# Kernel tuning notes

Hardware: AMD Instinct MI355X
Metric: run time of the kernel (lower is better)

Reference implementation:

```python
import jax, jax.numpy as jnp
import numpy as np
import math

V, E, H, L, HID, T, B = 32000, 1024, 16, 4, 4096, 1024, 4
HS = E // H  # head size = 64


def _ln(x, g, b, eps=1e-5):
    m = jnp.mean(x, axis=-1, keepdims=True)
    v = jnp.var(x, axis=-1, keepdims=True)
    return (x - m) * jax.lax.rsqrt(v + eps) * g + b


def _pos_encoding(t, e):
    pos = jnp.arange(t, dtype=jnp.float32)[:, None]
    div = jnp.exp(jnp.arange(0, e, 2, dtype=jnp.float32) * (-math.log(10000.0) / e))
    pe = jnp.zeros((t, e), dtype=jnp.float32)
    pe = pe.at[:, 0::2].set(jnp.sin(pos * div))
    pe = pe.at[:, 1::2].set(jnp.cos(pos * div))
    return pe


def setup_inputs() -> dict:
    key = jax.random.key(0)
    ks = jax.random.split(key, 16)
    std = 0.02
    inp = {
        'idx': jax.random.randint(ks[0], (B, T), 0, V),
        'targets': jax.random.randint(ks[1], (B, T), 0, V),
        'tok_emb': jax.random.normal(ks[2], (V, E), jnp.float32) * std,
        'ln1_g': jnp.ones((L, E), jnp.float32),
        'ln1_b': jnp.zeros((L, E), jnp.float32),
        'wq': jax.random.normal(ks[3], (L, H, E, HS), jnp.float32) * std,
        'wk': jax.random.normal(ks[4], (L, H, E, HS), jnp.float32) * std,
        'wv': jax.random.normal(ks[5], (L, H, E, HS), jnp.float32) * std,
        'wo': jax.random.normal(ks[6], (L, H * HS, E), jnp.float32) * std,
        'bo': jnp.zeros((L, E), jnp.float32),
        'ln2_g': jnp.ones((L, E), jnp.float32),
        'ln2_b': jnp.zeros((L, E), jnp.float32),
        'w1': jax.random.normal(ks[7], (L, E, HID), jnp.float32) * std,
        'b1': jnp.zeros((L, HID), jnp.float32),
        'w2': jax.random.normal(ks[8], (L, HID, E), jnp.float32) * std,
        'b2': jnp.zeros((L, E), jnp.float32),
        'lnf_g': jnp.ones((E,), jnp.float32),
        'lnf_b': jnp.zeros((E,), jnp.float32),
        'lm_w': jax.random.normal(ks[9], (E, V), jnp.float32) * std,
        'lm_b': jnp.zeros((V,), jnp.float32),
    }
    return inp


def _forward(idx, targets, tok_emb, ln1_g, ln1_b, wq, wk, wv, wo, bo,
             ln2_g, ln2_b, w1, b1, w2, b2, lnf_g, lnf_b, lm_w, lm_b):
    b, t = idx.shape
    x = tok_emb[idx] * math.sqrt(E)              # [B,T,E], scaled embedding
    x = x + _pos_encoding(t, E)                  # sinusoidal pos enc
    causal = jnp.tril(jnp.ones((t, t), dtype=bool))
    scale = HS ** -0.5
    for l in range(L):
        h = _ln(x, ln1_g[l], ln1_b[l])
        q = jnp.einsum('bte,hek->bhtk', h, wq[l])
        k = jnp.einsum('bte,hek->bhtk', h, wk[l])
        v = jnp.einsum('bte,hek->bhtk', h, wv[l])
        scores = jnp.einsum('bhtk,bhsk->bhts', q, k) * scale
        scores = jnp.where(causal, scores, -jnp.inf)
        w = jax.nn.softmax(scores, axis=-1)
        o = jnp.einsum('bhts,bhsk->bhtk', w, v)
        o = o.transpose(0, 2, 1, 3).reshape(b, t, H * HS)  # concat heads
        x = x + o @ wo[l] + bo[l]
        h2 = _ln(x, ln2_g[l], ln2_b[l])
        x = x + jax.nn.relu(h2 @ w1[l] + b1[l]) @ w2[l] + b2[l]
    x = _ln(x, lnf_g, lnf_b)
    logits = x @ lm_w + lm_b                     # [B,T,V]
    logp = jax.nn.log_softmax(logits, axis=-1)
    loss = -jnp.mean(jnp.take_along_axis(logp, targets[..., None], axis=-1))
    return logits, loss


def reference(idx, targets, tok_emb, ln1_g, ln1_b, wq, wk, wv, wo, bo,
              ln2_g, ln2_b, w1, b1, w2, b2, lnf_g, lnf_b, lm_w, lm_b):
    return _forward(idx, targets, tok_emb, ln1_g, ln1_b, wq, wk, wv, wo, bo,
                    ln2_g, ln2_b, w1, b1, w2, b2, lnf_g, lnf_b, lm_w, lm_b)
```

## Files before the change

### kernel.cpp

```cpp
#include <hip/hip_runtime.h>
#include <hip/hip_bf16.h>
#include <math.h>

#define BB 4
#define TT 1024
#define BT 4096
#define EE 1024
#define HH 16
#define HSZ 64
#define LL 4
#define HID 4096
#define VV 32000
#define LOG2E 1.44269504f

typedef __attribute__((ext_vector_type(8))) __bf16 bf16x8;
typedef __attribute__((ext_vector_type(4))) float f32x4;

#define MFMA16(a, b, c) __builtin_amdgcn_mfma_f32_16x16x32_bf16((a), (b), (c), 0, 0, 0)

__device__ __forceinline__ int swz32(int row, int chunk) {
    return row * 32 + ((chunk ^ ((row >> 1) & 3)) << 3);
}

__device__ __forceinline__ void gload16(const __bf16* g, __bf16* l) {
    __builtin_amdgcn_global_load_lds(
        (const __attribute__((address_space(1))) unsigned int*)g,
        (__attribute__((address_space(3))) unsigned int*)l, 16, 0, 0);
}

__global__ __launch_bounds__(256) void transpose_conv(
    const float* __restrict__ in, __bf16* __restrict__ out,
    int R, int C, long ibs, int bdiv, long os1, long os2)
{
    __shared__ __bf16 tile[64][65];
    const int t = threadIdx.x;
    const int c0 = blockIdx.x * 64, r0 = blockIdx.y * 64;
    const int batch = blockIdx.z;
    const float* ib = in + (size_t)batch * ibs;
    __bf16* ob = out + (size_t)(batch / bdiv) * os1 + (size_t)(batch % bdiv) * os2;
#pragma unroll
    for (int p = 0; p < 4; ++p) {
        const int r = (t >> 4) + p * 16;
        const int c = (t & 15) * 4;
        float4 v = *(const float4*)(ib + (size_t)(r0 + r) * C + c0 + c);
        tile[c + 0][r] = (__bf16)v.x;
        tile[c + 1][r] = (__bf16)v.y;
        tile[c + 2][r] = (__bf16)v.z;
        tile[c + 3][r] = (__bf16)v.w;
    }
    __syncthreads();
#pragma unroll
    for (int p = 0; p < 2; ++p) {
        const int g = t + p * 256;
        const int co = g >> 3, ch = g & 7;
        bf16x8 vv;
#pragma unroll
        for (int j = 0; j < 8; ++j) vv[j] = tile[co][ch * 8 + j];
        *(bf16x8*)(ob + (size_t)(c0 + co) * R + r0 + ch * 8) = vv;
    }
}

__global__ __launch_bounds__(256) void embed_kernel(
    const int* __restrict__ idx, const float* __restrict__ emb, float* __restrict__ x)
{
    const int row = blockIdx.x, tid = threadIdx.x;
    const float pos = (float)(row & (TT - 1));
    const int tok = idx[row];
    const int cb = tid * 4;
    float4 ev = *(const float4*)(emb + (size_t)tok * EE + cb);
    const float kk = -9.2103403720f / (float)EE;
    float pe[4];
#pragma unroll
    for (int j = 0; j < 4; ++j) {
        const int c = cb + j;
        const float div = expf(kk * (float)(c & ~1));
        const float ang = pos * div;
        pe[j] = (c & 1) ? cosf(ang) : sinf(ang);
    }
    float4 r;
    r.x = ev.x * 32.0f + pe[0];
    r.y = ev.y * 32.0f + pe[1];
    r.z = ev.z * 32.0f + pe[2];
    r.w = ev.w * 32.0f + pe[3];
    *(float4*)(x + (size_t)row * EE + cb) = r;
}

__global__ __launch_bounds__(256) void ln_kernel(
    const float* __restrict__ x, const float* __restrict__ g,
    const float* __restrict__ be, __bf16* __restrict__ out)
{
    __shared__ float red[2][4];
    const int row = blockIdx.x, tid = threadIdx.x;
    float4 v = *(const float4*)(x + (size_t)row * EE + tid * 4);
    float s = v.x + v.y + v.z + v.w;
    float ss = v.x * v.x + v.y * v.y + v.z * v.z + v.w * v.w;
#pragma unroll
    for (int m = 1; m < 64; m <<= 1) { s += __shfl_xor(s, m); ss += __shfl_xor(ss, m); }
    if ((tid & 63) == 0) { red[0][tid >> 6] = s; red[1][tid >> 6] = ss; }
    __syncthreads();
    s  = red[0][0] + red[0][1] + red[0][2] + red[0][3];
    ss = red[1][0] + red[1][1] + red[1][2] + red[1][3];
    const float mean = s * (1.0f / EE);
    const float var  = ss * (1.0f / EE) - mean * mean;
    const float rs   = rsqrtf(var + 1e-5f);
    float4 gv = *(const float4*)(g + tid * 4);
    float4 bv = *(const float4*)(be + tid * 4);
    __bf16* o = out + (size_t)row * EE + tid * 4;
    o[0] = (__bf16)((v.x - mean) * rs * gv.x + bv.x);
    o[1] = (__bf16)((v.y - mean) * rs * gv.y + bv.y);
    o[2] = (__bf16)((v.z - mean) * rs * gv.z + bv.z);
    o[3] = (__bf16)((v.w - mean) * rs * gv.w + bv.w);
}

template <int MODE, int GSWZ, int BN>
__global__ __launch_bounds__(256, 2) void gemm_bt(
    const __bf16* __restrict__ A, const __bf16* __restrict__ Bt,
    const float* __restrict__ bias, float* __restrict__ C,
    __bf16* __restrict__ Cb, float2* __restrict__ part,
    int M, int N, int K)
{
    constexpr int JW  = BN / 32;
    constexpr int BSW = BN / 64;
    __shared__ __bf16 As[128 * 32];
    __shared__ __bf16 Bs[BN * 32];
    __shared__ float2 red[(MODE == 4) ? 128 : 1][2];

    const int tid = threadIdx.x;
    const int lane = tid & 63, wid = tid >> 6;
    const int wr = wid >> 1, wc = wid & 1;
    int bm, bn;
    if (GSWZ) {
        const int b = blockIdx.x;
        const int j = b >> 3;
        bm = (b & 7) * 4 + (j & 3);
        bn = j >> 2;
    } else {
        bm = blockIdx.y; bn = blockIdx.x;
    }
    const int m0 = bm * 128, n0 = bn * BN;

    size_t sA[2];  int loA[2];
#pragma unroll
    for (int c = 0; c < 2; ++c) {
        const int seg = wid * 2 + c;
        const int rl = seg * 16 + (lane >> 2);
        const int cl = (lane & 3) ^ ((rl >> 1) & 3);
        loA[c] = seg * 512;
        sA[c] = (size_t)(m0 + rl) * K + cl * 8;
    }
    size_t sB[BSW]; int loB[BSW];
#pragma unroll
    for (int c = 0; c < BSW; ++c) {
        const int seg = wid * BSW + c;
        const int rl = seg * 16 + (lane >> 2);
        const int cl = (lane & 3) ^ ((rl >> 1) & 3);
        loB[c] = seg * 512;
        sB[c] = (size_t)(n0 + rl) * K + cl * 8;
    }

    const int l15 = lane & 15, kch = lane >> 4;
    const int abase = swz32(wr * 64 + l15, kch);
    const int bbase = swz32(wc * (BN / 2) + l15, kch);

    f32x4 acc[4][JW] = {};

    const int nk = K >> 5;
    for (int kt = 0; kt < nk; ++kt) {
        const size_t ko = (size_t)kt * 32;
#pragma unroll
        for (int c = 0; c < 2; ++c)   gload16(A + sA[c] + ko, As + loA[c]);
#pragma unroll
        for (int c = 0; c < BSW; ++c) gload16(Bt + sB[c] + ko, Bs + loB[c]);
        __syncthreads();
        bf16x8 af[4], bfr[JW];
#pragma unroll
        for (int i = 0; i < 4; ++i)  af[i]  = *(const bf16x8*)(As + abase + i * 512);
#pragma unroll
        for (int j = 0; j < JW; ++j) bfr[j] = *(const bf16x8*)(Bs + bbase + j * 512);
#pragma unroll
        for (int i = 0; i < 4; ++i)
#pragma unroll
            for (int j = 0; j < JW; ++j)
                acc[i][j] = MFMA16(af[i], bfr[j], acc[i][j]);
        __syncthreads();
    }

    const int crow = m0 + wr * 64 + ((lane >> 4) << 2);
    const int ccol = n0 + wc * (BN / 2) + l15;
#pragma unroll
    for (int i = 0; i < 4; ++i)
#pragma unroll
        for (int j = 0; j < JW; ++j) {
            const int cc = ccol + j * 16;
#pragma unroll
            for (int r = 0; r < 4; ++r) {
                const size_t oidx = (size_t)(crow + i * 16 + r) * N + cc;
                float v = acc[i][j][r];
                if (MODE == 0) {
                    Cb[oidx] = (__bf16)v;
                } else if (MODE == 1) {
                    v += bias[cc];
                    Cb[oidx] = (__bf16)(v > 0.0f ? v : 0.0f);
                } else if (MODE == 2) {
                    C[oidx] += v + bias[cc];
                } else {
                    __builtin_nontemporal_store(v + bias[cc], &C[oidx]);
                }
            }
        }

    if constexpr (MODE == 4) {
        const int lg = lane >> 4;
#pragma unroll
        for (int i = 0; i < 4; ++i)
#pragma unroll
            for (int r = 0; r < 4; ++r) {
                float tv[4];
                float mx = -1e30f;
#pragma unroll
                for (int j = 0; j < 4; ++j) {
                    tv[j] = acc[i][j][r] + bias[ccol + j * 16];
                    mx = fmaxf(mx, tv[j]);
                }
                mx = fmaxf(mx, __shfl_xor(mx, 1));
                mx = fmaxf(mx, __shfl_xor(mx, 2));
                mx = fmaxf(mx, __shfl_xor(mx, 4));
                mx = fmaxf(mx, __shfl_xor(mx, 8));
                float sm = 0.0f;
#pragma unroll
                for (int j = 0; j < 4; ++j) sm += exp2f((tv[j] - mx) * LOG2E);
                sm += __shfl_xor(sm, 1);
                sm += __shfl_xor(sm, 2);
                sm += __shfl_xor(sm, 4);
                sm += __shfl_xor(sm, 8);
                if (l15 == 0)
                    red[wr * 64 + i * 16 + lg * 4 + r][wc] = make_float2(mx, sm);
            }
        __syncthreads();
        if (tid < 128) {
            const float2 a = red[tid][0], b = red[tid][1];
            const float M2 = fmaxf(a.x, b.x);
            const float S = a.y * exp2f((a.x - M2) * LOG2E)
                          + b.y * exp2f((b.x - M2) * LOG2E);
            part[(size_t)(m0 + tid) * (N >> 7) + bn] = make_float2(M2, S);
        }
    }
}

__global__ __launch_bounds__(64) void attn_kernel(
    const __bf16* __restrict__ qkv, __bf16* __restrict__ out)
{
    __shared__ __bf16 Pl[16 * 32];
    __shared__ __bf16 Vt[64 * 32];
    const int lane = threadIdx.x;
    const int bh = blockIdx.x, b = bh >> 4, hh = bh & 15;
    const int qbase = blockIdx.y * 16;
    const int RS = 3 * EE;
    const __bf16* qp = qkv + (size_t)(b * TT) * RS + hh * HSZ;
    const __bf16* kp = qp + EE;
    const __bf16* vp = qp + 2 * EE;
    const int l15 = lane & 15, lg = lane >> 4;

    bf16x8 aq[2];
#pragma unroll
    for (int e = 0; e < 2; ++e)
        aq[e] = *(const bf16x8*)(qp + (size_t)(qbase + l15) * RS + e * 32 + lg * 8);

    f32x4 ao[4] = {};
    float mrun[4], lrun[4];
#pragma unroll
    for (int r = 0; r < 4; ++r) { mrun[r] = -1e30f; lrun[r] = 0.0f; }

    const int ntile = qbase / 32 + 1;
    for (int st = 0; st < ntile; ++st) {
        const int sbase = st * 32;
        f32x4 as[2] = {};
        __builtin_amdgcn_s_setprio(1);
#pragma unroll
        for (int n = 0; n < 2; ++n)
#pragma unroll
            for (int e = 0; e < 2; ++e) {
                bf16x8 bk = *(const bf16x8*)(kp + (size_t)(sbase + n * 16 + l15) * RS + e * 32 + lg * 8);
                as[n] = MFMA16(aq[e], bk, as[n]);
            }
        __builtin_amdgcn_s_setprio(0);
        {
            const int sl = lane >> 1;
            const int e0 = (lane & 1) * 32;
            const __bf16* vr = vp + (size_t)(sbase + sl) * RS + e0;
#pragma unroll
            for (int c = 0; c < 4; ++c) {
                bf16x8 vvv = *(const bf16x8*)(vr + c * 8);
#pragma unroll
                for (int j = 0; j < 8; ++j)
                    Vt[swz32(e0 + c * 8 + j, sl >> 3) + (sl & 7)] = vvv[j];
            }
        }
#pragma unroll
        for (int r = 0; r < 4; ++r) {
            const int qi = qbase + lg * 4 + r;
            float sc0 = as[0][r] * 0.125f;
            float sc1 = as[1][r] * 0.125f;
            if (sbase + l15 > qi)      sc0 = -1e30f;
            if (sbase + 16 + l15 > qi) sc1 = -1e30f;
            float rm = fmaxf(sc0, sc1);
            rm = fmaxf(rm, __shfl_xor(rm, 1));
            rm = fmaxf(rm, __shfl_xor(rm, 2));
            rm = fmaxf(rm, __shfl_xor(rm, 4));
            rm = fmaxf(rm, __shfl_xor(rm, 8));
            const float mnew = fmaxf(mrun[r], rm);
            const float alpha = exp2f((mrun[r] - mnew) * LOG2E);
            const float p0 = exp2f((sc0 - mnew) * LOG2E);
            const float p1 = exp2f((sc1 - mnew) * LOG2E);
            float rs = p0 + p1;
            rs += __shfl_xor(rs, 1);
            rs += __shfl_xor(rs, 2);
            rs += __shfl_xor(rs, 4);
            rs += __shfl_xor(rs, 8);
            lrun[r] = lrun[r] * alpha + rs;
            mrun[r] = mnew;
#pragma unroll
            for (int n = 0; n < 4; ++n) ao[n][r] *= alpha;
            const int prow = lg * 4 + r;
            Pl[swz32(prow, l15 >> 3) + (l15 & 7)] = (__bf16)p0;
            Pl[swz32(prow, (16 + l15) >> 3) + (l15 & 7)] = (__bf16)p1;
        }
        asm volatile("s_waitcnt lgkmcnt(0)" ::: "memory");
        bf16x8 pa = *(const bf16x8*)(&Pl[swz32(l15, lg)]);
        __builtin_amdgcn_s_setprio(1);
#pragma unroll
        for (int n = 0; n < 4; ++n) {
            bf16x8 bv = *(const bf16x8*)(&Vt[swz32(n * 16 + l15, lg)]);
            ao[n] = MFMA16(pa, bv, ao[n]);
        }
        __builtin_amdgcn_s_setprio(0);
        asm volatile("s_waitcnt lgkmcnt(0)" ::: "memory");
    }
#pragma unroll
    for (int r = 0; r < 4; ++r) {
        const float inv = 1.0f / lrun[r];
        const int row = qbase + lg * 4 + r;
#pragma unroll
        for (int n = 0; n < 4; ++n)
            out[(size_t)(b * TT + row) * EE + hh * HSZ + n * 16 + l15] =
                (__bf16)(ao[n][r] * inv);
    }
}

__global__ __launch_bounds__(256) void loss_reduce(
    const float2* __restrict__ part, const float* __restrict__ logits,
    const int* __restrict__ tgt, float* __restrict__ lossv)
{
    __shared__ float rm[4], rs2[4];
    const int row = blockIdx.x, tid = threadIdx.x;
    float m = -1e30f, s = 0.0f;
    if (tid < (VV >> 7)) {
        const float2 p = part[(size_t)row * (VV >> 7) + tid];
        m = p.x; s = p.y;
    }
#pragma unroll
    for (int k = 1; k < 64; k <<= 1) {
        const float mo = __shfl_xor(m, k), so = __shfl_xor(s, k);
        const float mn = fmaxf(m, mo);
        s = s * exp2f((m - mn) * LOG2E) + so * exp2f((mo - mn) * LOG2E);
        m = mn;
    }
    if ((tid & 63) == 0) { rm[tid >> 6] = m; rs2[tid >> 6] = s; }
    __syncthreads();
    if (tid == 0) {
        float M = rm[0];
#pragma unroll
        for (int w = 1; w < 4; ++w) M = fmaxf(M, rm[w]);
        float S = 0.0f;
#pragma unroll
        for (int w = 0; w < 4; ++w) S += rs2[w] * exp2f((rm[w] - M) * LOG2E);
        lossv[row] = M + logf(S) - logits[(size_t)row * VV + tgt[row]];
    }
}

__global__ __launch_bounds__(256) void loss_final(const float* __restrict__ lossv, float* __restrict__ out)
{
    __shared__ float red[4];
    const int tid = threadIdx.x;
    float s = 0.0f;
    for (int i = tid; i < BT; i += 256) s += lossv[i];
#pragma unroll
    for (int k = 1; k < 64; k <<= 1) s += __shfl_xor(s, k);
    if ((tid & 63) == 0) red[tid >> 6] = s;
    __syncthreads();
    if (tid == 0) out[0] = (red[0] + red[1] + red[2] + red[3]) * (1.0f / BT);
}

extern "C" void kernel_launch(void* const* d_in, const int* in_sizes, int n_in,
                              void* d_out, int out_size, void* d_ws, size_t ws_size,
                              hipStream_t stream)
{
    const int*   idx   = (const int*)d_in[0];
    const int*   tgt   = (const int*)d_in[1];
    const float* temb  = (const float*)d_in[2];
    const float* ln1g  = (const float*)d_in[3];
    const float* ln1b  = (const float*)d_in[4];
    const float* wq    = (const float*)d_in[5];
    const float* wk    = (const float*)d_in[6];
    const float* wv    = (const float*)d_in[7];
    const float* wo    = (const float*)d_in[8];
    const float* bo    = (const float*)d_in[9];
    const float* ln2g  = (const float*)d_in[10];
    const float* ln2b  = (const float*)d_in[11];
    const float* w1    = (const float*)d_in[12];
    const float* b1    = (const float*)d_in[13];
    const float* w2    = (const float*)d_in[14];
    const float* b2    = (const float*)d_in[15];
    const float* lnfg  = (const float*)d_in[16];
    const float* lnfb  = (const float*)d_in[17];
    const float* lm_w  = (const float*)d_in[18];
    const float* lm_b  = (const float*)d_in[19];

    float* logits  = (float*)d_out;
    float* lossout = logits + (size_t)BT * VV;

    char* ws = (char*)d_ws;
    size_t off = 0;
    auto carve = [&](size_t bytes) {
        void* p = ws + off;
        off += (bytes + 255) & ~(size_t)255;
        return p;
    };
    __bf16* WQKVT = (__bf16*)carve((size_t)LL * 3072 * 1024 * 2);
    __bf16* WOT   = (__bf16*)carve((size_t)LL * 1024 * 1024 * 2);
    __bf16* W1T   = (__bf16*)carve((size_t)LL * 4096 * 1024 * 2);
    __bf16* W2T   = (__bf16*)carve((size_t)LL * 1024 * 4096 * 2);
    __bf16* LMT   = (__bf16*)carve((size_t)VV * 1024 * 2);
    float*  x     = (float*)carve((size_t)BT * EE * 4);
    __bf16* h     = (__bf16*)carve((size_t)BT * EE * 2);
    __bf16* qkv   = (__bf16*)carve((size_t)BT * 3072 * 2);
    __bf16* mid   = (__bf16*)carve((size_t)BT * HID * 2);
    float*  lossv = (float*)carve((size_t)BT * 4);
    float2* part  = (float2*)mid;

    const dim3 blk(256);

    transpose_conv<<<dim3(1, 16, 64), blk, 0, stream>>>(wq, WQKVT,           1024, 64,   65536, 16, 3145728, 65536);
    transpose_conv<<<dim3(1, 16, 64), blk, 0, stream>>>(wk, WQKVT + 1048576, 1024, 64,   65536, 16, 3145728, 65536);
    transpose_conv<<<dim3(1, 16, 64), blk, 0, stream>>>(wv, WQKVT + 2097152, 1024, 64,   65536, 16, 3145728, 65536);
    transpose_conv<<<dim3(16, 16, 4), blk, 0, stream>>>(wo, WOT,   1024, 1024, 1048576, 4, 0, 1048576);
    transpose_conv<<<dim3(64, 16, 4), blk, 0, stream>>>(w1, W1T,   1024, 4096, 4194304, 4, 0, 4194304);
    transpose_conv<<<dim3(16, 64, 4), blk, 0, stream>>>(w2, W2T,   4096, 1024, 4194304, 4, 0, 4194304);
    transpose_conv<<<dim3(500, 16, 1), blk, 0, stream>>>(lm_w, LMT, 1024, 32000, 0, 1, 0, 0);

    embed_kernel<<<BT, blk, 0, stream>>>(idx, temb, x);

    for (int l = 0; l < LL; ++l) {
        ln_kernel<<<BT, blk, 0, stream>>>(x, ln1g + l * EE, ln1b + l * EE, h);
        gemm_bt<0, 0, 128><<<dim3(24, 32), blk, 0, stream>>>(h, WQKVT + (size_t)l * 3145728,
                                                             nullptr, nullptr, qkv, nullptr, BT, 3072, 1024);
        attn_kernel<<<dim3(64, 64), dim3(64), 0, stream>>>(qkv, h);
        gemm_bt<2, 0, 64><<<dim3(16, 32), blk, 0, stream>>>(h, WOT + (size_t)l * 1048576,
                                                            bo + l * EE, x, nullptr, nullptr, BT, 1024, 1024);
        ln_kernel<<<BT, blk, 0, stream>>>(x, ln2g + l * EE, ln2b + l * EE, h);
        gemm_bt<1, 0, 128><<<dim3(32, 32), blk, 0, stream>>>(h, W1T + (size_t)l * 4194304,
                                                             b1 + l * HID, nullptr, mid, nullptr, BT, 4096, 1024);
        gemm_bt<2, 0, 64><<<dim3(16, 32), blk, 0, stream>>>(mid, W2T + (size_t)l * 4194304,
                                                            b2 + l * EE, x, nullptr, nullptr, BT, 1024, 4096);
    }
    ln_kernel<<<BT, blk, 0, stream>>>(x, lnfg, lnfb, h);
    gemm_bt<4, 1, 128><<<dim3(8000), blk, 0, stream>>>(h, LMT, lm_b, logits, nullptr, part, BT, VV, 1024);
    loss_reduce<<<BT, blk, 0, stream>>>(part, logits, tgt, lossv);
    loss_final<<<1, blk, 0, stream>>>(lossv, lossout);
}
```

Baseline: 1.644 ms.

## Write V transposed from QKV GEMM epilogue and use lazy softmax rescaling in attention

The QKV GEMM gains a mode that writes the V columns straight into a per-head transposed [b,h,e,t] buffer. The attention kernel can then load V fragments directly from global memory instead of transposing them through shared memory on every tile. The attention softmax now rescales the running max only when the new max exceeds the old by more than a threshold, which skips most exp and multiply work on the accumulators. The logits store also drops its nontemporal hint. Costs are strided 8-byte scattered stores in the GEMM epilogue, uncoalesced global V reads in attention, and a wider range for unnormalized exponentials.

Measured after the change: 1.675 ms. About the same (+1.8%).

```diff
diff --git a/kernel.cpp b/kernel.cpp
--- a/kernel.cpp
+++ b/kernel.cpp
@@ -116,8 +116,8 @@
 __global__ __launch_bounds__(256, 2) void gemm_bt(
     const __bf16* __restrict__ A, const __bf16* __restrict__ Bt,
     const float* __restrict__ bias, float* __restrict__ C,
-    __bf16* __restrict__ Cb, float2* __restrict__ part,
-    int M, int N, int K)
+    __bf16* __restrict__ Cb, __bf16* __restrict__ Vx,
+    float2* __restrict__ part, int M, int N, int K)
 {
     constexpr int JW  = BN / 32;
     constexpr int BSW = BN / 64;
@@ -187,27 +187,58 @@
 
     const int crow = m0 + wr * 64 + ((lane >> 4) << 2);
     const int ccol = n0 + wc * (BN / 2) + l15;
-#pragma unroll
-    for (int i = 0; i < 4; ++i)
-#pragma unroll
-        for (int j = 0; j < JW; ++j) {
-            const int cc = ccol + j * 16;
-#pragma unroll
-            for (int r = 0; r < 4; ++r) {
-                const size_t oidx = (size_t)(crow + i * 16 + r) * N + cc;
-                float v = acc[i][j][r];
-                if (MODE == 0) {
-                    Cb[oidx] = (__bf16)v;
-                } else if (MODE == 1) {
-                    v += bias[cc];
-                    Cb[oidx] = (__bf16)(v > 0.0f ? v : 0.0f);
-                } else if (MODE == 2) {
-                    C[oidx] += v + bias[cc];
-                } else {
-                    __builtin_nontemporal_store(v + bias[cc], &C[oidx]);
+
+    if constexpr (MODE == 5) {
+        if (n0 >= 2048) {
+#pragma unroll
+            for (int i = 0; i < 4; ++i) {
+                const int t0 = crow + i * 16;
+                const int bb = t0 >> 10, tl = t0 & 1023;
+#pragma unroll
+                for (int j = 0; j < JW; ++j) {
+                    const int cc = ccol + j * 16;
+                    const int hh2 = (cc - 2048) >> 6;
+                    const int e = cc & 63;
+                    alignas(8) __bf16 tmp[4];
+#pragma unroll
+                    for (int r = 0; r < 4; ++r) tmp[r] = (__bf16)acc[i][j][r];
+                    *(uint2*)(Vx + ((((size_t)bb * HH + hh2) * HSZ + e) << 10) + tl) =
+                        *(const uint2*)tmp;
                 }
             }
+        } else {
+#pragma unroll
+            for (int i = 0; i < 4; ++i)
+#pragma unroll
+                for (int j = 0; j < JW; ++j)
+#pragma unroll
+                    for (int r = 0; r < 4; ++r)
+                        Cb[(size_t)(crow + i * 16 + r) * N + ccol + j * 16] =
+                            (__bf16)acc[i][j][r];
         }
+    } else {
+#pragma unroll
+        for (int i = 0; i < 4; ++i)
+#pragma unroll
+            for (int j = 0; j < JW; ++j) {
+                const int cc = ccol + j * 16;
+#pragma unroll
+                for (int r = 0; r < 4; ++r) {
+                    const size_t oidx = (size_t)(crow + i * 16 + r) * N + cc;
+                    float v = acc[i][j][r];
+                    if (MODE == 0) {
+                        Cb[oidx] = (__bf16)v;
+                    } else if (MODE == 1) {
+                        v += bias[cc];
+                        Cb[oidx] = (__bf16)(v > 0.0f ? v : 0.0f);
+                    } else if (MODE == 2) {
+                        C[oidx] += v + bias[cc];
+                    } else {
+                        C[oidx] = v + bias[cc];
+                    }
+                }
+            }
+    }
 
     if constexpr (MODE == 4) {
         const int lg = lane >> 4;
@@ -248,17 +279,17 @@
 }
 
 __global__ __launch_bounds__(64) void attn_kernel(
-    const __bf16* __restrict__ qkv, __bf16* __restrict__ out)
+    const __bf16* __restrict__ qkv, const __bf16* __restrict__ vT,
+    __bf16* __restrict__ out)
 {
     __shared__ __bf16 Pl[16 * 32];
-    __shared__ __bf16 Vt[64 * 32];
     const int lane = threadIdx.x;
     const int bh = blockIdx.x, b = bh >> 4, hh = bh & 15;
     const int qbase = blockIdx.y * 16;
     const int RS = 3 * EE;
     const __bf16* qp = qkv + (size_t)(b * TT) * RS + hh * HSZ;
     const __bf16* kp = qp + EE;
-    const __bf16* vp = qp + 2 * EE;
+    const __bf16* vp = vT + ((size_t)(b * HH + hh) << 16);
     const int l15 = lane & 15, lg = lane >> 4;
 
     bf16x8 aq[2];
@@ -284,18 +315,6 @@
                 as[n] = MFMA16(aq[e], bk, as[n]);
             }
         __builtin_amdgcn_s_setprio(0);
-        {
-            const int sl = lane >> 1;
-            const int e0 = (lane & 1) * 32;
-            const __bf16* vr = vp + (size_t)(sbase + sl) * RS + e0;
-#pragma unroll
-            for (int c = 0; c < 4; ++c) {
-                bf16x8 vvv = *(const bf16x8*)(vr + c * 8);
-#pragma unroll
-                for (int j = 0; j < 8; ++j)
-                    Vt[swz32(e0 + c * 8 + j, sl >> 3) + (sl & 7)] = vvv[j];
-            }
-        }
 #pragma unroll
         for (int r = 0; r < 4; ++r) {
             const int qi = qbase + lg * 4 + r;
@@ -308,19 +327,21 @@
             rm = fmaxf(rm, __shfl_xor(rm, 2));
             rm = fmaxf(rm, __shfl_xor(rm, 4));
             rm = fmaxf(rm, __shfl_xor(rm, 8));
-            const float mnew = fmaxf(mrun[r], rm);
-            const float alpha = exp2f((mrun[r] - mnew) * LOG2E);
-            const float p0 = exp2f((sc0 - mnew) * LOG2E);
-            const float p1 = exp2f((sc1 - mnew) * LOG2E);
+            if (rm > mrun[r] + 8.0f) {
+                const float alpha = exp2f((mrun[r] - rm) * LOG2E);
+                lrun[r] *= alpha;
+#pragma unroll
+                for (int n = 0; n < 4; ++n) ao[n][r] *= alpha;
+                mrun[r] = rm;
+            }
+            const float p0 = exp2f((sc0 - mrun[r]) * LOG2E);
+            const float p1 = exp2f((sc1 - mrun[r]) * LOG2E);
             float rs = p0 + p1;
             rs += __shfl_xor(rs, 1);
             rs += __shfl_xor(rs, 2);
             rs += __shfl_xor(rs, 4);
             rs += __shfl_xor(rs, 8);
-            lrun[r] = lrun[r] * alpha + rs;
-            mrun[r] = mnew;
-#pragma unroll
-            for (int n = 0; n < 4; ++n) ao[n][r] *= alpha;
+            lrun[r] += rs;
             const int prow = lg * 4 + r;
             Pl[swz32(prow, l15 >> 3) + (l15 & 7)] = (__bf16)p0;
             Pl[swz32(prow, (16 + l15) >> 3) + (l15 & 7)] = (__bf16)p1;
@@ -330,11 +351,10 @@
         __builtin_amdgcn_s_setprio(1);
 #pragma unroll
         for (int n = 0; n < 4; ++n) {
-            bf16x8 bv = *(const bf16x8*)(&Vt[swz32(n * 16 + l15, lg)]);
+            bf16x8 bv = *(const bf16x8*)(vp + ((n * 16 + l15) << 10) + sbase + lg * 8);
             ao[n] = MFMA16(pa, bv, ao[n]);
         }
         __builtin_amdgcn_s_setprio(0);
-        asm volatile("s_waitcnt lgkmcnt(0)" ::: "memory");
     }
 #pragma unroll
     for (int r = 0; r < 4; ++r) {
@@ -349,13 +369,13 @@
 
 __global__ __launch_bounds__(256) void loss_reduce(
     const float2* __restrict__ part, const float* __restrict__ logits,
-    const int* __restrict__ tgt, float* __restrict__ lossv)
+    const int* __restrict__ tgt, float* __restrict__ lossv, int NP)
 {
     __shared__ float rm[4], rs2[4];
     const int row = blockIdx.x, tid = threadIdx.x;
     float m = -1e30f, s = 0.0f;
-    if (tid < (VV >> 7)) {
-        const float2 p = part[(size_t)row * (VV >> 7) + tid];
+    if (tid < NP) {
+        const float2 p = part[(size_t)row * NP + tid];
         m = p.x; s = p.y;
     }
 #pragma unroll
@@ -434,6 +454,7 @@
     float*  x     = (float*)carve((size_t)BT * EE * 4);
     __bf16* h     = (__bf16*)carve((size_t)BT * EE * 2);
     __bf16* qkv   = (__bf16*)carve((size_t)BT * 3072 * 2);
+    __bf16* vT    = (__bf16*)carve((size_t)BB * HH * HSZ * TT * 2);
     __bf16* mid   = (__bf16*)carve((size_t)BT * HID * 2);
     float*  lossv = (float*)carve((size_t)BT * 4);
     float2* part  = (float2*)mid;
@@ -452,19 +473,20 @@
 
     for (int l = 0; l < LL; ++l) {
         ln_kernel<<<BT, blk, 0, stream>>>(x, ln1g + l * EE, ln1b + l * EE, h);
-        gemm_bt<0, 0, 128><<<dim3(24, 32), blk, 0, stream>>>(h, WQKVT + (size_t)l * 3145728,
-                                                             nullptr, nullptr, qkv, nullptr, BT, 3072, 1024);
-        attn_kernel<<<dim3(64, 64), dim3(64), 0, stream>>>(qkv, h);
+        gemm_bt<5, 0, 128><<<dim3(24, 32), blk, 0, stream>>>(h, WQKVT + (size_t)l * 3145728,
+            nullptr, nullptr, qkv, vT, nullptr, BT, 3072, 1024);
+        attn_kernel<<<dim3(64, 64), dim3(64), 0, stream>>>(qkv, vT, h);
         gemm_bt<2, 0, 64><<<dim3(16, 32), blk, 0, stream>>>(h, WOT + (size_t)l * 1048576,
-                                                            bo + l * EE, x, nullptr, nullptr, BT, 1024, 1024);
+            bo + l * EE, x, nullptr, nullptr, nullptr, BT, 1024, 1024);
         ln_kernel<<<BT, blk, 0, stream>>>(x, ln2g + l * EE, ln2b + l * EE, h);
         gemm_bt<1, 0, 128><<<dim3(32, 32), blk, 0, stream>>>(h, W1T + (size_t)l * 4194304,
-                                                             b1 + l * HID, nullptr, mid, nullptr, BT, 4096, 1024);
+            b1 + l * HID, nullptr, mid, nullptr, nullptr, BT, 4096, 1024);
         gemm_bt<2, 0, 64><<<dim3(16, 32), blk, 0, stream>>>(mid, W2T + (size_t)l * 4194304,
-                                                            b2 + l * EE, x, nullptr, nullptr, BT, 1024, 4096);
+            b2 + l * EE, x, nullptr, nullptr, nullptr, BT, 1024, 4096);
     }
     ln_kernel<<<BT, blk, 0, stream>>>(x, lnfg, lnfb, h);
-    gemm_bt<4, 1, 128><<<dim3(8000), blk, 0, stream>>>(h, LMT, lm_b, logits, nullptr, part, BT, VV, 1024);
-    loss_reduce<<<BT, blk, 0, stream>>>(part, logits, tgt, lossv);
+    gemm_bt<4, 1, 128><<<dim3(8000), blk, 0, stream>>>(h, LMT, lm_b, logits,
+        nullptr, nullptr, part, BT, VV, 1024);
+    loss_reduce<<<BT, blk, 0, stream>>>(part, logits, tgt, lossv, VV >> 7);
     loss_final<<<1, blk, 0, stream>>>(lossv, lossout);
 }
```
